# Kernel optimization log

Measured on AMD Instinct MI355X. Metric: run time of the kernel, lower is better.

Reference implementation:

```python
import jax, jax.numpy as jnp
import numpy as np

B, C, T, H, W, E, K = 2, 256, 16, 32, 32, 4, 2


def setup_inputs() -> dict:
    key = jax.random.key(0)
    ks = jax.random.split(key, 5)
    x = jax.random.normal(ks[0], (B, C, T, H, W), dtype=jnp.float32)
    # gate: Conv3d(dim, E, 1) -> weight [E, C], bias [E]
    gate_w = jax.random.normal(ks[1], (E, C), dtype=jnp.float32) * 0.02
    gate_b = jnp.zeros((E,), dtype=jnp.float32)
    # experts_layer1: Conv3d(dim, dim*E, 1) -> weight [E*C, C], bias [E*C]
    w1 = jax.random.normal(ks[2], (E * C, C), dtype=jnp.float32) * 0.02
    b1 = jnp.zeros((E * C,), dtype=jnp.float32)
    # experts_layer2: Conv3d(dim*E, dim*E, 1, groups=E) -> per-expert [C, C]
    w2 = jax.random.normal(ks[3], (E, C, C), dtype=jnp.float32) * 0.02
    b2 = jnp.zeros((E, C), dtype=jnp.float32)
    return {"x": x, "gate_w": gate_w, "gate_b": gate_b,
            "w1": w1, "b1": b1, "w2": w2, "b2": b2}


def reference(x, gate_w, gate_b, w1, b1, w2, b2):
    # gating: 1x1x1 conv == channel contraction; logits [B,T,H,W,E]
    logits = jnp.einsum('bcthw,ec->bthwe', x, gate_w) + gate_b
    vals, idx = jax.lax.top_k(logits, K)              # [B,T,H,W,K]
    wk = jax.nn.softmax(vals, axis=-1).astype(x.dtype)
    # scatter top-k softmax weights back into E slots (zeros elsewhere)
    weights = jnp.sum(jax.nn.one_hot(idx, E, dtype=x.dtype) * wk[..., None],
                      axis=-2)                        # [B,T,H,W,E]
    # layer1 (dense 1x1x1 conv) + SiLU; output channels = E*C
    h = jax.nn.silu(jnp.einsum('bcthw,oc->bothw', x, w1)
                    + b1[None, :, None, None, None])
    h = h.reshape(B, E, C, T, H, W)
    # layer2: grouped 1x1x1 conv, one [C,C] matmul per expert
    expert_out = (jnp.einsum('becthw,eoc->beothw', h, w2)
                  + b2[None, :, :, None, None, None])  # [B,E,C,T,H,W]
    # weighted combine over experts + residual
    out = jnp.einsum('becthw,bthwe->bcthw', expert_out, weights)
    return out + x
```

## Files before the change

kernel.cpp:

```cpp
#include <hip/hip_runtime.h>
#include <hip/hip_bf16.h>


#define C_DIM 256
#define S_DIM 16384
#define E_DIM 4
#define MT 64
#define XST 264
#define WFRAG_ELEMS 262144

typedef __attribute__((ext_vector_type(8))) short bf16x8;
typedef __attribute__((ext_vector_type(4))) float f32x4;

__global__ __launch_bounds__(256) void prepack_kernel(
    const float* __restrict__ w1, const float* __restrict__ w2,
    __hip_bfloat16* __restrict__ dst)
{
  int o = blockIdx.x * 256 + threadIdx.x;
  int half = o >> 18;
  int idx = o & (WFRAG_ELEMS - 1);
  int j    = idx & 7;
  int lane = (idx >> 3) & 63;
  int kc   = (idx >> 9) & 7;
  int nt   = (idx >> 12) & 15;
  int e    = (idx >> 16) & 3;
  const float* src = half ? w2 : w1;
  int si = (e*256 + nt*16 + (lane & 15))*256 + kc*32 + (lane >> 4)*8 + j;
  dst[o] = __float2bfloat16(src[si]);
}

__global__ __launch_bounds__(256, 2) void moe_fused_kernel(
    const float* __restrict__ x,
    const float* __restrict__ gate_w,
    const float* __restrict__ gate_b,
    const float* __restrict__ b1,
    const float* __restrict__ b2,
    const __hip_bfloat16* __restrict__ wp,
    float* __restrict__ out)
{
  __shared__ __align__(16) __hip_bfloat16 Xs[MT * XST];
  __shared__ __align__(16) __hip_bfloat16 Hs[MT * XST];
  __shared__ float Wgt[MT * 4];

  const int tid  = threadIdx.x;
  const int lane = tid & 63;
  const int wv   = tid >> 6;
  const int r    = lane & 15;
  const int q    = lane >> 4;

  const int g  = blockIdx.x;
  const int b  = g >> 8;
  const int s0 = (g & 255) * MT;
  const float* xb = x + (size_t)b * C_DIM * S_DIM + s0;

  {
    const int p4 = (tid & 15) * 4;
    const int c0 = tid >> 4;
#pragma unroll
    for (int cc = 0; cc < 16; ++cc) {
      const int c = cc * 16 + c0;
      const float4 v = *(const float4*)(xb + (size_t)c * S_DIM + p4);
      Xs[(p4+0)*XST + c] = __float2bfloat16(v.x);
      Xs[(p4+1)*XST + c] = __float2bfloat16(v.y);
      Xs[(p4+2)*XST + c] = __float2bfloat16(v.z);
      Xs[(p4+3)*XST + c] = __float2bfloat16(v.w);
    }
  }

  {
    const int p = lane;
    const int e = wv;
    const float* gw = gate_w + e * C_DIM;
    const float* xr = xb + p;
    double a0 = 0.0, a1 = 0.0, a2 = 0.0, a3 = 0.0;
#pragma unroll 4
    for (int c = 0; c < C_DIM; c += 4) {
      a0 += (double)xr[(size_t)(c+0) * S_DIM] * (double)gw[c+0];
      a1 += (double)xr[(size_t)(c+1) * S_DIM] * (double)gw[c+1];
      a2 += (double)xr[(size_t)(c+2) * S_DIM] * (double)gw[c+2];
      a3 += (double)xr[(size_t)(c+3) * S_DIM] * (double)gw[c+3];
    }
    Wgt[p*4 + e] = (float)(((a0 + a1) + (a2 + a3)) + (double)gate_b[e]);
  }
  __syncthreads();

  if (tid < MT) {
    const int p = tid;
    const float l0 = Wgt[p*4+0], l1 = Wgt[p*4+1], l2 = Wgt[p*4+2], l3 = Wgt[p*4+3];
    int i1 = 0; float v1 = l0;
    if (l1 > v1) { v1 = l1; i1 = 1; }
    if (l2 > v1) { v1 = l2; i1 = 2; }
    if (l3 > v1) { v1 = l3; i1 = 3; }
    float v2 = -3.0e38f; int i2 = 0;
    if (i1 != 0 && l0 > v2) { v2 = l0; i2 = 0; }
    if (i1 != 1 && l1 > v2) { v2 = l1; i2 = 1; }
    if (i1 != 2 && l2 > v2) { v2 = l2; i2 = 2; }
    if (i1 != 3 && l3 > v2) { v2 = l3; i2 = 3; }
    const float wA = 1.0f / (1.0f + __expf(v2 - v1));
    const float wB = 1.0f - wA;
    Wgt[p*4+0] = (i1 == 0) ? wA : ((i2 == 0) ? wB : 0.0f);
    Wgt[p*4+1] = (i1 == 1) ? wA : ((i2 == 1) ? wB : 0.0f);
    Wgt[p*4+2] = (i1 == 2) ? wA : ((i2 == 2) ? wB : 0.0f);
    Wgt[p*4+3] = (i1 == 3) ? wA : ((i2 == 3) ? wB : 0.0f);
  }
  __syncthreads();

  const short* XsS = (const short*)Xs;
  short*       HsW = (short*)Hs;
  const short* HsR = (const short*)Hs;
  const short* W1P = (const short*)wp;
  const short* W2P = (const short*)wp + WFRAG_ELEMS;

  f32x4 oacc[4][4];
#pragma unroll
  for (int i = 0; i < 4; ++i)
#pragma unroll
    for (int j = 0; j < 4; ++j) oacc[i][j] = (f32x4){0.f, 0.f, 0.f, 0.f};

  for (int e = 0; e < E_DIM; ++e) {
    f32x4 hacc[4][4];
#pragma unroll
    for (int i = 0; i < 4; ++i)
#pragma unroll
      for (int j = 0; j < 4; ++j) hacc[i][j] = (f32x4){0.f, 0.f, 0.f, 0.f};

    {
      const short* w1e = W1P + ((e*16 + wv*4)*8)*512 + lane*8;
      bf16x8 bw[4], bwn[4];
#pragma unroll
      for (int t = 0; t < 4; ++t)
        bw[t] = *(const bf16x8*)(w1e + (t*8 + 0)*512);
#pragma unroll
      for (int kc = 0; kc < 8; ++kc) {
        if (kc < 7) {
#pragma unroll
          for (int t = 0; t < 4; ++t)
            bwn[t] = *(const bf16x8*)(w1e + (t*8 + kc + 1)*512);
        }
        bf16x8 a[4];
#pragma unroll
        for (int Mt = 0; Mt < 4; ++Mt)
          a[Mt] = *(const bf16x8*)(XsS + (Mt*16 + r)*XST + kc*32 + q*8);
#pragma unroll
        for (int Mt = 0; Mt < 4; ++Mt)
#pragma unroll
          for (int t = 0; t < 4; ++t)
            hacc[Mt][t] = __builtin_amdgcn_mfma_f32_16x16x32_bf16(a[Mt], bw[t], hacc[Mt][t], 0, 0, 0);
#pragma unroll
        for (int t = 0; t < 4; ++t) bw[t] = bwn[t];
      }
    }

    {
      float wreg[4][4];
#pragma unroll
      for (int Mt = 0; Mt < 4; ++Mt)
#pragma unroll
        for (int reg = 0; reg < 4; ++reg)
          wreg[Mt][reg] = Wgt[(Mt*16 + q*4 + reg)*4 + e];
#pragma unroll
      for (int t = 0; t < 4; ++t) {
        const int n = wv*64 + t*16 + r;
        const float bias = b1[e*256 + n];
#pragma unroll
        for (int Mt = 0; Mt < 4; ++Mt)
#pragma unroll
          for (int reg = 0; reg < 4; ++reg) {
            const float z = hacc[Mt][t][reg] + bias;
            const float h = z / (1.0f + __expf(-z)) * wreg[Mt][reg];
            __hip_bfloat16 hb = __float2bfloat16(h);
            HsW[(Mt*16 + q*4 + reg)*XST + n] = *(short*)&hb;
          }
      }
    }
    __syncthreads();

    {
      const short* w2e = W2P + ((e*16 + wv*4)*8)*512 + lane*8;
      bf16x8 bw[4], bwn[4];
#pragma unroll
      for (int t = 0; t < 4; ++t)
        bw[t] = *(const bf16x8*)(w2e + (t*8 + 0)*512);
#pragma unroll
      for (int kc = 0; kc < 8; ++kc) {
        if (kc < 7) {
#pragma unroll
          for (int t = 0; t < 4; ++t)
            bwn[t] = *(const bf16x8*)(w2e + (t*8 + kc + 1)*512);
        }
        bf16x8 a[4];
#pragma unroll
        for (int Mt = 0; Mt < 4; ++Mt)
          a[Mt] = *(const bf16x8*)(HsR + (Mt*16 + r)*XST + kc*32 + q*8);
#pragma unroll
        for (int Mt = 0; Mt < 4; ++Mt)
#pragma unroll
          for (int t = 0; t < 4; ++t)
            oacc[Mt][t] = __builtin_amdgcn_mfma_f32_16x16x32_bf16(a[Mt], bw[t], oacc[Mt][t], 0, 0, 0);
#pragma unroll
        for (int t = 0; t < 4; ++t) bw[t] = bwn[t];
      }
    }
    __syncthreads();
  }

  float b2v[4][4];
#pragma unroll
  for (int t = 0; t < 4; ++t) {
    const int c = wv*64 + t*16 + r;
#pragma unroll
    for (int e = 0; e < 4; ++e) b2v[t][e] = b2[e*256 + c];
  }

  float* ob = out + (size_t)b * C_DIM * S_DIM + s0;
#pragma unroll
  for (int Mt = 0; Mt < 4; ++Mt)
#pragma unroll
    for (int reg = 0; reg < 4; ++reg) {
      const int p = Mt*16 + q*4 + reg;
      const float w0 = Wgt[p*4+0], w1 = Wgt[p*4+1], w2 = Wgt[p*4+2], w3 = Wgt[p*4+3];
#pragma unroll
      for (int t = 0; t < 4; ++t) {
        const int c = wv*64 + t*16 + r;
        const float wsum = w0*b2v[t][0] + w1*b2v[t][1] + w2*b2v[t][2] + w3*b2v[t][3];
        ob[(size_t)c * S_DIM + p] = oacc[Mt][t][reg] + wsum + xb[(size_t)c * S_DIM + p];
      }
    }
}

extern "C" void kernel_launch(void* const* d_in, const int* in_sizes, int n_in,
                              void* d_out, int out_size, void* d_ws, size_t ws_size,
                              hipStream_t stream)
{
  (void)in_sizes; (void)n_in; (void)out_size; (void)ws_size;
  const float* x      = (const float*)d_in[0];
  const float* gate_w = (const float*)d_in[1];
  const float* gate_b = (const float*)d_in[2];
  const float* w1     = (const float*)d_in[3];
  const float* b1     = (const float*)d_in[4];
  const float* w2     = (const float*)d_in[5];
  const float* b2     = (const float*)d_in[6];
  float* out = (float*)d_out;
  __hip_bfloat16* wpack = (__hip_bfloat16*)d_ws;

  prepack_kernel<<<2048, 256, 0, stream>>>(w1, w2, wpack);
  moe_fused_kernel<<<512, 256, 0, stream>>>(x, gate_w, gate_b, b1, b2, wpack, out);
}
```

Baseline: 149.5 us.

## Stage output through LDS for coalesced stores and deepen weight prefetch

```diff
diff --git a/kernel.cpp b/kernel.cpp
--- a/kernel.cpp
+++ b/kernel.cpp
@@ -7,10 +7,17 @@
 #define E_DIM 4
 #define MT 64
 #define XST 264
+#define OST 68
 #define WFRAG_ELEMS 262144
 
 typedef __attribute__((ext_vector_type(8))) short bf16x8;
+typedef __attribute__((ext_vector_type(4))) short short4v;
 typedef __attribute__((ext_vector_type(4))) float f32x4;
+
+__device__ __forceinline__ short bfq(float f) {
+  __hip_bfloat16 h = __float2bfloat16(f);
+  return *(short*)&h;
+}
 
 __global__ __launch_bounds__(256) void prepack_kernel(
     const float* __restrict__ w1, const float* __restrict__ w2,
@@ -38,9 +45,12 @@
     const __hip_bfloat16* __restrict__ wp,
     float* __restrict__ out)
 {
-  __shared__ __align__(16) __hip_bfloat16 Xs[MT * XST];
-  __shared__ __align__(16) __hip_bfloat16 Hs[MT * XST];
+  __shared__ __align__(16) char pool[256 * OST * 4];
   __shared__ float Wgt[MT * 4];
+
+  short* XsS = (short*)pool;
+  short* HsS = (short*)(pool + MT * XST * 2);
+  float* Os  = (float*)pool;
 
   const int tid  = threadIdx.x;
   const int lane = tid & 63;
@@ -55,15 +65,18 @@
 
   {
     const int p4 = (tid & 15) * 4;
-    const int c0 = tid >> 4;
-#pragma unroll
-    for (int cc = 0; cc < 16; ++cc) {
-      const int c = cc * 16 + c0;
-      const float4 v = *(const float4*)(xb + (size_t)c * S_DIM + p4);
-      Xs[(p4+0)*XST + c] = __float2bfloat16(v.x);
-      Xs[(p4+1)*XST + c] = __float2bfloat16(v.y);
-      Xs[(p4+2)*XST + c] = __float2bfloat16(v.z);
-      Xs[(p4+3)*XST + c] = __float2bfloat16(v.w);
+    const int cg = tid >> 4;
+#pragma unroll
+    for (int cc = 0; cc < 4; ++cc) {
+      const int c0 = (cc*16 + cg) * 4;
+      const float4 v0 = *(const float4*)(xb + (size_t)(c0+0)*S_DIM + p4);
+      const float4 v1 = *(const float4*)(xb + (size_t)(c0+1)*S_DIM + p4);
+      const float4 v2 = *(const float4*)(xb + (size_t)(c0+2)*S_DIM + p4);
+      const float4 v3 = *(const float4*)(xb + (size_t)(c0+3)*S_DIM + p4);
+      *(short4v*)(XsS + (p4+0)*XST + c0) = (short4v){bfq(v0.x), bfq(v1.x), bfq(v2.x), bfq(v3.x)};
+      *(short4v*)(XsS + (p4+1)*XST + c0) = (short4v){bfq(v0.y), bfq(v1.y), bfq(v2.y), bfq(v3.y)};
+      *(short4v*)(XsS + (p4+2)*XST + c0) = (short4v){bfq(v0.z), bfq(v1.z), bfq(v2.z), bfq(v3.z)};
+      *(short4v*)(XsS + (p4+3)*XST + c0) = (short4v){bfq(v0.w), bfq(v1.w), bfq(v2.w), bfq(v3.w)};
     }
   }
 
@@ -105,9 +118,6 @@
   }
   __syncthreads();
 
-  const short* XsS = (const short*)Xs;
-  short*       HsW = (short*)Hs;
-  const short* HsR = (const short*)Hs;
   const short* W1P = (const short*)wp;
   const short* W2P = (const short*)wp + WFRAG_ELEMS;
 
@@ -126,16 +136,17 @@
 
     {
       const short* w1e = W1P + ((e*16 + wv*4)*8)*512 + lane*8;
-      bf16x8 bw[4], bwn[4];
-#pragma unroll
-      for (int t = 0; t < 4; ++t)
-        bw[t] = *(const bf16x8*)(w1e + (t*8 + 0)*512);
+      bf16x8 bw[3][4];
+#pragma unroll
+      for (int t = 0; t < 4; ++t) bw[0][t] = *(const bf16x8*)(w1e + (t*8 + 0)*512);
+#pragma unroll
+      for (int t = 0; t < 4; ++t) bw[1][t] = *(const bf16x8*)(w1e + (t*8 + 1)*512);
 #pragma unroll
       for (int kc = 0; kc < 8; ++kc) {
-        if (kc < 7) {
-#pragma unroll
-          for (int t = 0; t < 4; ++t)
-            bwn[t] = *(const bf16x8*)(w1e + (t*8 + kc + 1)*512);
+        if (kc < 6) {
+#pragma unroll
+          for (int t = 0; t < 4; ++t)
+            bw[(kc+2)%3][t] = *(const bf16x8*)(w1e + (t*8 + kc + 2)*512);
         }
         bf16x8 a[4];
 #pragma unroll
@@ -145,11 +156,16 @@
         for (int Mt = 0; Mt < 4; ++Mt)
 #pragma unroll
           for (int t = 0; t < 4; ++t)
-            hacc[Mt][t] = __builtin_amdgcn_mfma_f32_16x16x32_bf16(a[Mt], bw[t], hacc[Mt][t], 0, 0, 0);
-#pragma unroll
-        for (int t = 0; t < 4; ++t) bw[t] = bwn[t];
-      }
-    }
+            hacc[Mt][t] = __builtin_amdgcn_mfma_f32_16x16x32_bf16(a[Mt], bw[kc%3][t], hacc[Mt][t], 0, 0, 0);
+      }
+    }
+
+    const short* w2e = W2P + ((e*16 + wv*4)*8)*512 + lane*8;
+    bf16x8 cw[3][4];
+#pragma unroll
+    for (int t = 0; t < 4; ++t) cw[0][t] = *(const bf16x8*)(w2e + (t*8 + 0)*512);
+#pragma unroll
+    for (int t = 0; t < 4; ++t) cw[1][t] = *(const bf16x8*)(w2e + (t*8 + 1)*512);
 
     {
       float wreg[4][4];
@@ -167,65 +183,78 @@
 #pragma unroll
           for (int reg = 0; reg < 4; ++reg) {
             const float z = hacc[Mt][t][reg] + bias;
-            const float h = z / (1.0f + __expf(-z)) * wreg[Mt][reg];
-            __hip_bfloat16 hb = __float2bfloat16(h);
-            HsW[(Mt*16 + q*4 + reg)*XST + n] = *(short*)&hb;
+            const float s = __builtin_amdgcn_rcpf(1.0f + __expf(-z));
+            const float h = z * s * wreg[Mt][reg];
+            HsS[(Mt*16 + q*4 + reg)*XST + n] = bfq(h);
           }
       }
     }
     __syncthreads();
 
     {
-      const short* w2e = W2P + ((e*16 + wv*4)*8)*512 + lane*8;
-      bf16x8 bw[4], bwn[4];
-#pragma unroll
-      for (int t = 0; t < 4; ++t)
-        bw[t] = *(const bf16x8*)(w2e + (t*8 + 0)*512);
 #pragma unroll
       for (int kc = 0; kc < 8; ++kc) {
-        if (kc < 7) {
-#pragma unroll
-          for (int t = 0; t < 4; ++t)
-            bwn[t] = *(const bf16x8*)(w2e + (t*8 + kc + 1)*512);
+        if (kc < 6) {
+#pragma unroll
+          for (int t = 0; t < 4; ++t)
+            cw[(kc+2)%3][t] = *(const bf16x8*)(w2e + (t*8 + kc + 2)*512);
         }
         bf16x8 a[4];
 #pragma unroll
         for (int Mt = 0; Mt < 4; ++Mt)
-          a[Mt] = *(const bf16x8*)(HsR + (Mt*16 + r)*XST + kc*32 + q*8);
-#pragma unroll
-        for (int Mt = 0; Mt < 4; ++Mt)
-#pragma unroll
-          for (int t = 0; t < 4; ++t)
-            oacc[Mt][t] = __builtin_amdgcn_mfma_f32_16x16x32_bf16(a[Mt], bw[t], oacc[Mt][t], 0, 0, 0);
-#pragma unroll
-        for (int t = 0; t < 4; ++t) bw[t] = bwn[t];
+          a[Mt] = *(const bf16x8*)(HsS + (Mt*16 + r)*XST + kc*32 + q*8);
+#pragma unroll
+        for (int Mt = 0; Mt < 4; ++Mt)
+#pragma unroll
+          for (int t = 0; t < 4; ++t)
+            oacc[Mt][t] = __builtin_amdgcn_mfma_f32_16x16x32_bf16(a[Mt], cw[kc%3][t], oacc[Mt][t], 0, 0, 0);
       }
     }
     __syncthreads();
   }
 
-  float b2v[4][4];
-#pragma unroll
-  for (int t = 0; t < 4; ++t) {
-    const int c = wv*64 + t*16 + r;
-#pragma unroll
-    for (int e = 0; e < 4; ++e) b2v[t][e] = b2[e*256 + c];
-  }
-
-  float* ob = out + (size_t)b * C_DIM * S_DIM + s0;
-#pragma unroll
-  for (int Mt = 0; Mt < 4; ++Mt)
-#pragma unroll
-    for (int reg = 0; reg < 4; ++reg) {
-      const int p = Mt*16 + q*4 + reg;
-      const float w0 = Wgt[p*4+0], w1 = Wgt[p*4+1], w2 = Wgt[p*4+2], w3 = Wgt[p*4+3];
+  {
+    float b2v[4][4];
+#pragma unroll
+    for (int t = 0; t < 4; ++t) {
+      const int c = wv*64 + t*16 + r;
+#pragma unroll
+      for (int e = 0; e < 4; ++e) b2v[t][e] = b2[e*256 + c];
+    }
+#pragma unroll
+    for (int Mt = 0; Mt < 4; ++Mt) {
+      f32x4 wv4[4];
+#pragma unroll
+      for (int reg = 0; reg < 4; ++reg)
+        wv4[reg] = *(const f32x4*)(&Wgt[(Mt*16 + q*4 + reg)*4]);
 #pragma unroll
       for (int t = 0; t < 4; ++t) {
-        const int c = wv*64 + t*16 + r;
-        const float wsum = w0*b2v[t][0] + w1*b2v[t][1] + w2*b2v[t][2] + w3*b2v[t][3];
-        ob[(size_t)c * S_DIM + p] = oacc[Mt][t][reg] + wsum + xb[(size_t)c * S_DIM + p];
-      }
-    }
+        f32x4 v = oacc[Mt][t];
+#pragma unroll
+        for (int reg = 0; reg < 4; ++reg)
+          v[reg] += wv4[reg][0]*b2v[t][0] + wv4[reg][1]*b2v[t][1]
+                  + wv4[reg][2]*b2v[t][2] + wv4[reg][3]*b2v[t][3];
+        *(f32x4*)(Os + (size_t)(wv*64 + t*16 + r)*OST + Mt*16 + q*4) = v;
+      }
+    }
+  }
+  __syncthreads();
+
+  {
+    const int p4 = (tid & 15) * 4;
+    const int cg = tid >> 4;
+    float* ob = out + (size_t)b * C_DIM * S_DIM + s0;
+#pragma unroll
+    for (int cc = 0; cc < 16; ++cc) {
+      const int c = cc*16 + cg;
+      const f32x4  o  = *(const f32x4*)(Os + (size_t)c*OST + p4);
+      const float4 xr = *(const float4*)(xb + (size_t)c*S_DIM + p4);
+      float4 res;
+      res.x = o[0] + xr.x; res.y = o[1] + xr.y;
+      res.z = o[2] + xr.z; res.w = o[3] + xr.w;
+      *(float4*)(ob + (size_t)c*S_DIM + p4) = res;
+    }
+  }
 }
 
 extern "C" void kernel_launch(void* const* d_in, const int* in_sizes, int n_in,
```

After: 146.8 us. About the same (-1.8%).
